# Optimization experiments

Hardware: AMD Instinct MI355X
Metric: run time of the kernel (lower is better)

The kernel has to match this reference:

```python
import math
import jax, jax.numpy as jnp
import numpy as np

B, T, E, H = 1, 2048, 2048, 16
D = E // H // 2  # head_dim = 64
DEPTH = 12
LAMBDA_INIT = 0.8 - 0.6 * math.exp(-0.3 * DEPTH)
EPS = 1e-5
NEG = -1e30


def rotary_cos_sin(seqlen, dim):
    # matches flash-attn RotaryEmbedding: inv_freq over even indices, base 10000
    inv_freq = 1.0 / (10000.0 ** (jnp.arange(0, dim, 2, dtype=jnp.float32) / dim))
    t = jnp.arange(seqlen, dtype=jnp.float32)
    freqs = jnp.outer(t, inv_freq)  # [T, D/2]
    return jnp.cos(freqs), jnp.sin(freqs)


def apply_rotary_interleaved(x, cos, sin):
    # x: [B, T, nH, D]; rotate interleaved pairs (x0,x1),(x2,x3),...
    x1 = x[..., 0::2]
    x2 = x[..., 1::2]
    c = cos[None, :, None, :]
    s = sin[None, :, None, :]
    o1 = x1 * c - x2 * s
    o2 = x1 * s + x2 * c
    return jnp.stack([o1, o2], axis=-1).reshape(x.shape)


def causal_attn_pair(q, k, v1, v2, mask, scale):
    # q,k,v*: [B, T, H, D]; shared softmax over (q,k), applied to both v1 and v2
    s = jnp.einsum('bthd,bshd->bhts', q, k) * scale
    s = jnp.where(mask, s, NEG)
    a = jax.nn.softmax(s, axis=-1)
    o1 = jnp.einsum('bhts,bshd->bthd', a, v1)
    o2 = jnp.einsum('bhts,bshd->bthd', a, v2)
    return jnp.concatenate([o1, o2], axis=-1)  # [B, T, H, 2D]


def setup_inputs() -> dict:
    key = jax.random.key(0)
    ks = jax.random.split(key, 10)
    return {
        'query': jax.random.normal(ks[0], (B, T, E), dtype=jnp.float32),
        'Wq': jax.random.normal(ks[1], (E, E), dtype=jnp.float32) * 0.02,
        'Wk': jax.random.normal(ks[2], (E, E), dtype=jnp.float32) * 0.02,
        'Wv': jax.random.normal(ks[3], (E, E), dtype=jnp.float32) * 0.02,
        'Wout': jax.random.normal(ks[4], (E, E), dtype=jnp.float32) * 0.02,
        'lambda_q1': jax.random.normal(ks[5], (D,), dtype=jnp.float32) * 0.1,
        'lambda_k1': jax.random.normal(ks[6], (D,), dtype=jnp.float32) * 0.1,
        'lambda_q2': jax.random.normal(ks[7], (D,), dtype=jnp.float32) * 0.1,
        'lambda_k2': jax.random.normal(ks[8], (D,), dtype=jnp.float32) * 0.1,
        'rms_weight': jnp.ones((2 * D,), dtype=jnp.float32),
    }


def reference(query, Wq, Wk, Wv, Wout, lambda_q1, lambda_k1, lambda_q2, lambda_k2, rms_weight):
    bsz, tgt_len, embed_dim = query.shape
    cos, sin = rotary_cos_sin(tgt_len, D)
    scale = D ** (-0.5)
    mask = jnp.tril(jnp.ones((tgt_len, tgt_len), dtype=bool))[None, None]

    q = (query @ Wq).reshape(bsz, tgt_len, 2 * H, D)
    k = (query @ Wk).reshape(bsz, tgt_len, 2 * H, D)
    v = (query @ Wv).reshape(bsz, tgt_len, H, 2, D)

    q = apply_rotary_emb = apply_rotary_interleaved(q, cos, sin)
    k = apply_rotary_interleaved(k, cos, sin)

    q = q.reshape(bsz, tgt_len, H, 2, D)
    k = k.reshape(bsz, tgt_len, H, 2, D)
    q1, q2 = q[:, :, :, 0], q[:, :, :, 1]
    k1, k2 = k[:, :, :, 0], k[:, :, :, 1]
    v1, v2 = v[:, :, :, 0], v[:, :, :, 1]

    attn1 = causal_attn_pair(q1, k1, v1, v2, mask, scale)  # [B,T,H,2D]
    attn2 = causal_attn_pair(q2, k2, v1, v2, mask, scale)

    lambda_1 = jnp.exp(jnp.sum(lambda_q1 * lambda_k1))
    lambda_2 = jnp.exp(jnp.sum(lambda_q2 * lambda_k2))
    lambda_full = lambda_1 - lambda_2 + LAMBDA_INIT

    f1 = jnp.fft.rfft(attn1, axis=1)
    f2 = jnp.fft.rfft(attn2, axis=1)
    attn_freq = f1 - lambda_full * f2

    n_freq = attn_freq.shape[1]
    sigma = 0.3 / 2.0  # cutoff_ratio / 2, gaussian window
    x = jnp.linspace(0.0, 1.0, n_freq)
    filt = jnp.exp(-0.5 * (x / sigma) ** 2)
    attn_freq = attn_freq * filt[None, :, None, None]

    attn = jnp.fft.irfft(attn_freq, n=tgt_len, axis=1)  # [B,T,H,2D]

    # RMSNorm over last dim (2*head_dim) with affine weight
    attn = attn * jax.lax.rsqrt(jnp.mean(attn * attn, axis=-1, keepdims=True) + EPS) * rms_weight
    attn = attn * (1.0 - LAMBDA_INIT)

    attn = attn.reshape(bsz, tgt_len, H * 2 * D)
    return attn @ Wout
```

## Files before the change

kernel.cpp:

```cpp
#include <hip/hip_runtime.h>
#include <math.h>

#define LAMBDA_INIT_F 0.7836057665316245f
#define ONE_MINUS_LI  0.2163942334683755f

typedef unsigned short ushort_t;
typedef unsigned int   uint32;
typedef unsigned long long u64;
typedef __attribute__((ext_vector_type(8))) short short8;
typedef __attribute__((ext_vector_type(4))) float f32x4;

__device__ __forceinline__ ushort_t f2bf(float f) {
    union { float f; uint32 u; } x; x.f = f;
    uint32 r = (x.u + 0x7fffu + ((x.u >> 16) & 1u)) >> 16;
    return (ushort_t)r;
}

__device__ __forceinline__ void gld16(ushort_t* lds, const ushort_t* g) {
    __builtin_amdgcn_global_load_lds(
        (const __attribute__((address_space(1))) uint32*)g,
        (__attribute__((address_space(3))) uint32*)lds,
        16, 0, 0);
}

__global__ __launch_bounds__(64) void lambda_kernel(
    const float* __restrict__ lq1, const float* __restrict__ lk1,
    const float* __restrict__ lq2, const float* __restrict__ lk2,
    float* __restrict__ lam)
{
    int l = threadIdx.x;
    float p1 = lq1[l] * lk1[l];
    float p2 = lq2[l] * lk2[l];
    for (int off = 32; off; off >>= 1) {
        p1 += __shfl_down(p1, off);
        p2 += __shfl_down(p2, off);
    }
    if (l == 0) lam[0] = expf(p1) - expf(p2) + LAMBDA_INIT_F;
}

__global__ __launch_bounds__(256) void gfilt_kernel(float* __restrict__ g)
{
    __shared__ float red[4];
    const int j = blockIdx.x;
    int tau = j - 64;
    int ta = tau < 0 ? -tau : tau;
    const int tid = threadIdx.x;
    float acc = 0.0f;
    for (int k = tid; k <= 1024; k += 256) {
        float w = (k == 0 || k == 1024) ? 1.0f : 2.0f;
        float r = (float)k * (1.0f / 153.6f);
        float f = expf(-0.5f * r * r);
        int m = (k * ta) & 2047;
        float ang = (float)m * 3.0679615757712823e-3f;
        acc += w * f * cosf(ang);
    }
    for (int off = 32; off; off >>= 1) acc += __shfl_down(acc, off);
    if ((tid & 63) == 0) red[tid >> 6] = acc;
    __syncthreads();
    if (tid == 0)
        g[j] = (red[0] + red[1] + red[2] + red[3]) * (1.0f / 2048.0f);
}

__global__ __launch_bounds__(256) void rottab(float* __restrict__ ct, float* __restrict__ st)
{
    int id = blockIdx.x * 256 + threadIdx.x;
    int t = id >> 5, i = id & 31;
    double inv = exp(-0.28782313662425575 * (double)i);
    double a = (double)t * inv;
    ct[id] = (float)cos(a);
    st[id] = (float)sin(a);
}

__global__ __launch_bounds__(256) void cvt_bf16(const float* __restrict__ s, ushort_t* __restrict__ d)
{
    int i = (blockIdx.x * 256 + threadIdx.x) * 8;
    float4 a = *(const float4*)(s + i);
    float4 b = *(const float4*)(s + i + 4);
    uint4 pk;
    pk.x = (uint32)f2bf(a.x) | ((uint32)f2bf(a.y) << 16);
    pk.y = (uint32)f2bf(a.z) | ((uint32)f2bf(a.w) << 16);
    pk.z = (uint32)f2bf(b.x) | ((uint32)f2bf(b.y) << 16);
    pk.w = (uint32)f2bf(b.z) | ((uint32)f2bf(b.w) << 16);
    *(uint4*)(d + i) = pk;
}

__global__ __launch_bounds__(256) void wtrans(
    const float* __restrict__ Wq, const float* __restrict__ Wk,
    const float* __restrict__ Wv, const float* __restrict__ Wo,
    ushort_t* __restrict__ Tq, ushort_t* __restrict__ Tk,
    ushort_t* __restrict__ Tv, ushort_t* __restrict__ To)
{
    int z = blockIdx.z;
    const float* S = (z == 0) ? Wq : (z == 1) ? Wk : (z == 2) ? Wv : Wo;
    ushort_t* Dt = (z == 0) ? Tq : (z == 1) ? Tk : (z == 2) ? Tv : To;
    bool perm = (z < 2);
    __shared__ float Ls[64 * 65];
    const int tid = threadIdx.x;
    const int n0 = blockIdx.x * 64, k0 = blockIdx.y * 64;
    #pragma unroll
    for (int it = 0; it < 4; ++it) {
        int kk = it * 16 + (tid >> 4);
        int nn = (tid & 15) * 4;
        float4 v = *(const float4*)(S + (size_t)(k0 + kk) * 2048 + n0 + nn);
        Ls[(nn + 0) * 65 + kk] = v.x;
        Ls[(nn + 1) * 65 + kk] = v.y;
        Ls[(nn + 2) * 65 + kk] = v.z;
        Ls[(nn + 3) * 65 + kk] = v.w;
    }
    __syncthreads();
    int nl = tid >> 2, kc = (tid & 3) * 16;
    int ng = n0 + nl;
    int nd = perm ? ((ng & ~63) | ((ng & 1) << 5) | ((ng & 63) >> 1)) : ng;
    uint4 p0, p1;
    const float* row = Ls + nl * 65 + kc;
    p0.x = (uint32)f2bf(row[0])  | ((uint32)f2bf(row[1])  << 16);
    p0.y = (uint32)f2bf(row[2])  | ((uint32)f2bf(row[3])  << 16);
    p0.z = (uint32)f2bf(row[4])  | ((uint32)f2bf(row[5])  << 16);
    p0.w = (uint32)f2bf(row[6])  | ((uint32)f2bf(row[7])  << 16);
    p1.x = (uint32)f2bf(row[8])  | ((uint32)f2bf(row[9])  << 16);
    p1.y = (uint32)f2bf(row[10]) | ((uint32)f2bf(row[11]) << 16);
    p1.z = (uint32)f2bf(row[12]) | ((uint32)f2bf(row[13]) << 16);
    p1.w = (uint32)f2bf(row[14]) | ((uint32)f2bf(row[15]) << 16);
    *(uint4*)(Dt + (size_t)nd * 2048 + k0 + kc) = p0;
    *(uint4*)(Dt + (size_t)nd * 2048 + k0 + kc + 8) = p1;
}

#define SB()    __builtin_amdgcn_s_barrier()
#define LGKM0() asm volatile("s_waitcnt lgkmcnt(0)" ::: "memory")
#define VM6()   asm volatile("s_waitcnt vmcnt(6)" ::: "memory")

__device__ __forceinline__ void rdA(short8 af[8], const ushort_t* Ah, int rbase, int quad)
{
    #pragma unroll
    for (int m = 0; m < 4; ++m) {
        int r = rbase + m * 16;
        #pragma unroll
        for (int ks = 0; ks < 2; ++ks)
            af[m * 2 + ks] = *(const short8*)(Ah + r * 64 + ((ks * 4 + quad) ^ (r & 7)) * 8);
    }
}
__device__ __forceinline__ void rdB(short8 bf[4], const ushort_t* Bh, int rbase, int quad)
{
    #pragma unroll
    for (int n = 0; n < 2; ++n) {
        int r = rbase + n * 32;
        #pragma unroll
        for (int ks = 0; ks < 2; ++ks)
            bf[n * 2 + ks] = *(const short8*)(Bh + r * 64 + ((ks * 4 + quad) ^ (r & 7)) * 8);
    }
}
template<int QA, int QB>
__device__ __forceinline__ void mfma16(const short8 af[8], const short8 bf[4], f32x4 acc[8][4])
{
    __builtin_amdgcn_s_setprio(1);
    #pragma unroll
    for (int m = 0; m < 4; ++m)
        #pragma unroll
        for (int n = 0; n < 2; ++n)
            #pragma unroll
            for (int ks = 0; ks < 2; ++ks)
                acc[QA * 4 + m][QB * 2 + n] = __builtin_amdgcn_mfma_f32_16x16x32_bf16(
                    af[m * 2 + ks], bf[n * 2 + ks], acc[QA * 4 + m][QB * 2 + n], 0, 0, 0);
    __builtin_amdgcn_s_setprio(0);
}

__global__ __launch_bounds__(512, 2) void gemm_qkv(
    const ushort_t* __restrict__ A, const ushort_t* __restrict__ WT,
    ushort_t* __restrict__ q1, ushort_t* __restrict__ q2,
    ushort_t* __restrict__ k1, ushort_t* __restrict__ k2,
    ushort_t* __restrict__ v1T, ushort_t* __restrict__ v2T,
    const float* __restrict__ ctab, const float* __restrict__ stab)
{
    __shared__ ushort_t sA0h0[8192], sA0h1[8192], sA1h0[8192], sA1h1[8192];
    __shared__ ushort_t sB0h0[8192], sB0h1[8192], sB1h0[8192], sB1h1[8192];
    const int tid = threadIdx.x;
    const int w = tid >> 6, lane = tid & 63;
    const int quad = lane >> 4, l15 = lane & 15;
    const int wr = w >> 2, wc = w & 3;
    const int rb = blockIdx.y * 256, cbg = blockIdx.x * 256;
    const int rA = wr * 64 + l15;
    const int rB = (wc >> 1) * 64 + (wc & 1) * 16 + l15;
    const int cib = w * 128;

    auto stA = [&](ushort_t* buf, int ha, int tau) {
        #pragma unroll
        for (int u = 0; u < 2; ++u) {
            int ci = cib + u * 64 + lane;
            int row = ci >> 3, cc = (ci & 7) ^ (row & 7);
            gld16(buf + (cib + u * 64) * 8,
                  A + (size_t)(rb + ha * 128 + row) * 2048 + tau * 64 + cc * 8);
        }
    };
    auto stB = [&](ushort_t* buf, int hb, int tau) {
        #pragma unroll
        for (int u = 0; u < 2; ++u) {
            int ci = cib + u * 64 + lane;
            int row = ci >> 3, cc = (ci & 7) ^ (row & 7);
            gld16(buf + (cib + u * 64) * 8,
                  WT + (size_t)(cbg + hb * 128 + row) * 2048 + tau * 64 + cc * 8);
        }
    };

    stA(sA0h0, 0, 0); stA(sA0h1, 1, 0); stB(sB0h0, 0, 0); stB(sB0h1, 1, 0);
    stA(sA1h0, 0, 1); stA(sA1h1, 1, 1); stB(sB1h0, 0, 1);

    f32x4 acc[8][4];
    #pragma unroll
    for (int i = 0; i < 8; ++i)
        #pragma unroll
        for (int j = 0; j < 4; ++j) acc[i][j] = (f32x4)0.0f;
    short8 af[8], bf[4];

    VM6();
    SB();

    for (int it = 0; it < 16; ++it) {
        const int t = it * 2;
        const int t1 = t + 1;
        const int t2 = (t + 2 < 32) ? t + 2 : 31;
        const int t3 = (t + 3 < 32) ? t + 3 : 31;
        rdA(af, sA0h0, rA, quad); rdB(bf, sB0h0, rB, quad);
        stB(sB1h1, 1, t1);
        SB(); LGKM0(); mfma16<0, 0>(af, bf, acc); SB();
        rdB(bf, sB0h1, rB, quad);
        stA(sA0h0, 0, t2);
        SB(); LGKM0(); mfma16<0, 1>(af, bf, acc); SB();
        rdA(af, sA0h1, rA, quad); rdB(bf, sB0h0, rB, quad);
        SB(); LGKM0(); mfma16<1, 0>(af, bf, acc); SB();
        rdB(bf, sB0h1, rB, quad);
        stA(sA0h1, 1, t2); stB(sB0h0, 0, t2);
        VM6();
        SB(); LGKM0(); mfma16<1, 1>(af, bf, acc); SB();
        rdA(af, sA1h0, rA, quad); rdB(bf, sB1h0, rB, quad);
        stB(sB0h1, 1, t2);
        SB(); LGKM0(); mfma16<0, 0>(af, bf, acc); SB();
        rdB(bf, sB1h1, rB, quad);
        stA(sA1h0, 0, t3);
        SB(); LGKM0(); mfma16<0, 1>(af, bf, acc); SB();
        rdA(af, sA1h1, rA, quad); rdB(bf, sB1h0, rB, quad);
        SB(); LGKM0(); mfma16<1, 0>(af, bf, acc); SB();
        rdB(bf, sB1h1, rB, quad);
        stA(sA1h1, 1, t3); stB(sB1h0, 0, t3);
        VM6();
        SB(); LGKM0(); mfma16<1, 1>(af, bf, acc); SB();
    }

    const int region = cbg >> 11;
    const int nloc = cbg & 2047;
    if (region < 2) {
        ushort_t* b1 = region ? k1 : q1;
        ushort_t* b2 = region ? k2 : q2;
        const int i = (wc & 1) * 16 + l15;
        #pragma unroll
        for (int qb = 0; qb < 2; ++qb) {
            int head2 = (nloc >> 6) + qb * 2 + (wc >> 1);
            ushort_t* dst = ((head2 & 1) ? b2 : b1) + (size_t)(head2 >> 1) * 2048 * 64;
            #pragma unroll
            for (int mi = 0; mi < 8; ++mi)
                #pragma unroll
                for (int r = 0; r < 4; ++r) {
                    int t = rb + (mi >> 2) * 128 + wr * 64 + (mi & 3) * 16 + quad * 4 + r;
                    float c = ctab[t * 32 + i], s = stab[t * 32 + i];
                    float x1 = acc[mi][qb * 2 + 0][r], x2 = acc[mi][qb * 2 + 1][r];
                    dst[(size_t)t * 64 + i]      = f2bf(x1 * c - x2 * s);
                    dst[(size_t)t * 64 + 32 + i] = f2bf(x1 * s + x2 * c);
                }
        }
    } else {
        #pragma unroll
        for (int mi = 0; mi < 8; ++mi)
            #pragma unroll
            for (int nj = 0; nj < 4; ++nj) {
                int cg = nloc + (nj >> 1) * 128 + (wc >> 1) * 64 + (wc & 1) * 16
                       + (nj & 1) * 32 + l15;
                int hh = cg >> 7, pr = (cg >> 6) & 1, d = cg & 63;
                int tb = rb + (mi >> 2) * 128 + wr * 64 + (mi & 3) * 16 + quad * 4;
                ushort_t* dst = (pr ? v2T : v1T) + ((size_t)(hh * 64 + d)) * 2048 + tb;
                u64 pk = (u64)f2bf(acc[mi][nj][0])
                       | ((u64)f2bf(acc[mi][nj][1]) << 16)
                       | ((u64)f2bf(acc[mi][nj][2]) << 32)
                       | ((u64)f2bf(acc[mi][nj][3]) << 48);
                *(u64*)dst = pk;
            }
    }
}

#define PSTRIDE 88

__device__ __forceinline__ void attn_step(
    const ushort_t* __restrict__ Kb, const ushort_t* __restrict__ V1b,
    const ushort_t* __restrict__ V2b, ushort_t* __restrict__ pw,
    const short8* qb, f32x4* O, float& m_i, float& l_i,
    int quad, int l15, int row_l, bool diag)
{
    f32x4 s[4];
    #pragma unroll
    for (int j = 0; j < 4; ++j) s[j] = (f32x4)0.0f;
    #pragma unroll
    for (int ks = 0; ks < 2; ++ks)
        #pragma unroll
        for (int j = 0; j < 4; ++j) {
            int r = j * 16 + l15;
            short8 kf = *(const short8*)(Kb + r * 64 + ((ks * 4 + quad) ^ (r & 7)) * 8);
            s[j] = __builtin_amdgcn_mfma_f32_16x16x32_bf16(kf, qb[ks], s[j], 0, 0, 0);
        }
    float mx = -1e30f;
    #pragma unroll
    for (int j = 0; j < 4; ++j)
        #pragma unroll
        for (int r = 0; r < 4; ++r) {
            float v = s[j][r] * 0.125f;
            if (diag) {
                int kp = j * 16 + quad * 4 + r;
                v = (kp <= row_l) ? v : -1e30f;
            }
            s[j][r] = v;
            mx = fmaxf(mx, v);
        }
    mx = fmaxf(mx, __shfl_xor(mx, 16));
    mx = fmaxf(mx, __shfl_xor(mx, 32));
    float newm = fmaxf(m_i, mx);
    float alpha = __expf(m_i - newm);
    float sum = 0.0f;
    #pragma unroll
    for (int j = 0; j < 4; ++j) {
        float p0 = __expf(s[j][0] - newm);
        float p1 = __expf(s[j][1] - newm);
        float p2 = __expf(s[j][2] - newm);
        float p3 = __expf(s[j][3] - newm);
        sum += (p0 + p1) + (p2 + p3);
        u64 pk = (u64)f2bf(p0) | ((u64)f2bf(p1) << 16)
               | ((u64)f2bf(p2) << 32) | ((u64)f2bf(p3) << 48);
        *(u64*)(pw + l15 * PSTRIDE + j * 16 + quad * 4) = pk;
    }
    sum += __shfl_xor(sum, 16);
    sum += __shfl_xor(sum, 32);
    l_i = l_i * alpha + sum;
    m_i = newm;
    float av0 = __shfl(alpha, quad * 4 + 0);
    float av1 = __shfl(alpha, quad * 4 + 1);
    float av2 = __shfl(alpha, quad * 4 + 2);
    float av3 = __shfl(alpha, quad * 4 + 3);
    #pragma unroll
    for (int nt = 0; nt < 8; ++nt) {
        O[nt][0] *= av0; O[nt][1] *= av1; O[nt][2] *= av2; O[nt][3] *= av3;
    }
    #pragma unroll
    for (int ks = 0; ks < 2; ++ks) {
        short8 pf = *(const short8*)(pw + l15 * PSTRIDE + ks * 32 + quad * 8);
        #pragma unroll
        for (int nt = 0; nt < 8; ++nt) {
            const ushort_t* Vs = (nt < 4) ? V1b : V2b;
            int d = (nt & 3) * 16 + l15;
            short8 vf = *(const short8*)(Vs + d * 64 + ((ks * 4 + quad) ^ (d & 7)) * 8);
            O[nt] = __builtin_amdgcn_mfma_f32_16x16x32_bf16(pf, vf, O[nt], 0, 0, 0);
        }
    }
}

__global__ __launch_bounds__(512, 4) void attn_pipe(
    const ushort_t* __restrict__ q1, const ushort_t* __restrict__ k1,
    const ushort_t* __restrict__ q2, const ushort_t* __restrict__ k2,
    const ushort_t* __restrict__ v1T, const ushort_t* __restrict__ v2T,
    float* __restrict__ X, const float* __restrict__ lam_ptr)
{
    __shared__ ushort_t Tt[4][4096];
    __shared__ ushort_t Ps[8][16 * PSTRIDE];

    const int tid = threadIdx.x;
    const int w = tid >> 6, lane = tid & 63;
    const int quad = lane >> 4, l15 = lane & 15;
    const int pair = w >> 2, wl = w & 3;
    const int b = blockIdx.x;
    const int h = b & 15;
    const int x16 = (b & 255) >> 4;
    const int qt = (b < 256) ? (31 - x16) : x16;
    const float lam = lam_ptr[0];
    const int row_l = wl * 16 + l15;

    const ushort_t* k1h = k1 + (size_t)h * 2048 * 64;
    const ushort_t* k2h = k2 + (size_t)h * 2048 * 64;
    const ushort_t* v1h = v1T + (size_t)h * 64 * 2048;
    const ushort_t* v2h = v2T + (size_t)h * 64 * 2048;

    short8 qb[2];
    {
        const ushort_t* qp = (pair ? q2 : q1)
            + ((size_t)h * 2048 + qt * 64 + wl * 16 + l15) * 64 + quad * 8;
        qb[0] = *(const short8*)(qp);
        qb[1] = *(const short8*)(qp + 32);
    }

    const int ci = tid;
    const int srow = ci >> 3, scc = (ci & 7) ^ (srow & 7);
    const int koff = srow * 64 + scc * 8;
    const int voff = srow * 2048 + scc * 8;

    short8 sK1, sK2, sV1, sV2;

    sK1 = *(const short8*)(k1h + koff);
    sK2 = *(const short8*)(k2h + koff);
    sV1 = *(const short8*)(v1h + voff);
    sV2 = *(const short8*)(v2h + voff);
    *(short8*)(&Tt[0][ci * 8]) = sK1;
    *(short8*)(&Tt[1][ci * 8]) = sK2;
    *(short8*)(&Tt[2][ci * 8]) = sV1;
    *(short8*)(&Tt[3][ci * 8]) = sV2;
    __syncthreads();

    f32x4 O[8];
    #pragma unroll
    for (int i = 0; i < 8; ++i) O[i] = (f32x4)0.0f;
    float m_i = -1e30f, l_i = 0.0f;

    const ushort_t* Kb = Tt[pair];

    for (int kt = 0; kt <= qt; ++kt) {
        if (kt < qt) {
            int kb = (kt + 1) * 4096, vb = (kt + 1) * 64;
            sK1 = *(const short8*)(k1h + kb + koff);
            sK2 = *(const short8*)(k2h + kb + koff);
            sV1 = *(const short8*)(v1h + vb + voff);
            sV2 = *(const short8*)(v2h + vb + voff);
        }
        attn_step(Kb, Tt[2], Tt[3], &Ps[w][0], qb, O, m_i, l_i,
                  quad, l15, row_l, kt == qt);
        __syncthreads();
        if (kt < qt) {
            *(short8*)(&Tt[0][ci * 8]) = sK1;
            *(short8*)(&Tt[1][ci * 8]) = sK2;
            *(short8*)(&Tt[2][ci * 8]) = sV1;
            *(short8*)(&Tt[3][ci * 8]) = sV2;
            __syncthreads();
        }
    }

    float sc = pair ? lam : 1.0f;
    float rr0 = sc / __shfl(l_i, quad * 4 + 0);
    float rr1 = sc / __shfl(l_i, quad * 4 + 1);
    float rr2 = sc / __shfl(l_i, quad * 4 + 2);
    float rr3 = sc / __shfl(l_i, quad * 4 + 3);

    float* LX = (float*)&Tt[0][0];
    const int rbase = wl * 16 + quad * 4;
    if (pair) {
        #pragma unroll
        for (int nt = 0; nt < 8; ++nt) {
            int cb = nt * 16 + l15;
            LX[(rbase + 0) * 128 + cb] = O[nt][0] * rr0;
            LX[(rbase + 1) * 128 + cb] = O[nt][1] * rr1;
            LX[(rbase + 2) * 128 + cb] = O[nt][2] * rr2;
            LX[(rbase + 3) * 128 + cb] = O[nt][3] * rr3;
        }
    }
    __syncthreads();
    if (!pair) {
        int tb = qt * 64 + rbase;
        #pragma unroll
        for (int nt = 0; nt < 8; ++nt) {
            int cb = nt * 16 + l15;
            int col = h * 128 + cb;
            X[(size_t)(tb + 0) * 2048 + col] = O[nt][0] * rr0 - LX[(rbase + 0) * 128 + cb];
            X[(size_t)(tb + 1) * 2048 + col] = O[nt][1] * rr1 - LX[(rbase + 1) * 128 + cb];
            X[(size_t)(tb + 2) * 2048 + col] = O[nt][2] * rr2 - LX[(rbase + 2) * 128 + cb];
            X[(size_t)(tb + 3) * 2048 + col] = O[nt][3] * rr3 - LX[(rbase + 3) * 128 + cb];
        }
    }
}

__global__ __launch_bounds__(256) void conv_t(
    const float* __restrict__ X, const float* __restrict__ g, float* __restrict__ Y)
{
    __shared__ float Xs[192 * 64];
    __shared__ float gs[129];
    const int tid = threadIdx.x;
    const int c0 = blockIdx.x * 64, t0 = blockIdx.y * 64;
    const int c = tid & 63, tg = tid >> 6;
    for (int j = tg; j < 192; j += 4)
        Xs[j * 64 + c] = X[(size_t)((t0 - 64 + j) & 2047) * 2048 + c0 + c];
    if (tid < 129) gs[tid] = g[tid];
    __syncthreads();
    float accv[16];
    #pragma unroll
    for (int i = 0; i < 16; ++i) accv[i] = 0.0f;
    const int tl0 = tg * 16;
    for (int tap = 0; tap < 129; ++tap) {
        float gv = gs[tap];
        int base = (tl0 + 128 - tap) * 64 + c;
        #pragma unroll
        for (int i = 0; i < 16; ++i) accv[i] += gv * Xs[base + i * 64];
    }
    #pragma unroll
    for (int i = 0; i < 16; ++i)
        Y[(size_t)(t0 + tl0 + i) * 2048 + c0 + c] = accv[i];
}

__global__ __launch_bounds__(64) void rms_bf(
    const float* __restrict__ Y, const float* __restrict__ wgt, ushort_t* __restrict__ yb)
{
    int grp = blockIdx.x;
    int t = grp >> 4, hh = grp & 15, l = threadIdx.x;
    size_t base = (size_t)t * 2048 + hh * 128;
    float a = Y[base + l];
    float b = Y[base + 64 + l];
    float ss = a * a + b * b;
    for (int off = 32; off; off >>= 1) ss += __shfl_down(ss, off);
    ss = __shfl(ss, 0);
    float r = rsqrtf(ss * (1.0f / 128.0f) + 1e-5f) * ONE_MINUS_LI;
    yb[base + l]      = f2bf(a * r * wgt[l]);
    yb[base + 64 + l] = f2bf(b * r * wgt[64 + l]);
}

__global__ __launch_bounds__(256) void gemm_out(
    const ushort_t* __restrict__ A, const ushort_t* __restrict__ BT,
    float* __restrict__ C)
{
    __shared__ ushort_t As[4096];
    __shared__ ushort_t Bs[8192];
    const int tid = threadIdx.x;
    const int w = tid >> 6, lane = tid & 63;
    const int quad = lane >> 4, l15 = lane & 15;
    const int wr = w >> 1, wc = w & 1;
    const int rb = blockIdx.y * 64, cb = blockIdx.x * 128;

    f32x4 acc[2][4];
    #pragma unroll
    for (int i = 0; i < 2; ++i)
        #pragma unroll
        for (int j = 0; j < 4; ++j) acc[i][j] = (f32x4)0.0f;

    for (int k0 = 0; k0 < 2048; k0 += 64) {
        #pragma unroll
        for (int u = 0; u < 2; ++u) {
            int off = (w * 2 + u) * 512;
            int Lc = (off >> 3) + lane;
            int row = Lc >> 3, cc = (Lc & 7) ^ (row & 7);
            gld16(As + off, A + (size_t)(rb + row) * 2048 + k0 + cc * 8);
        }
        #pragma unroll
        for (int u = 0; u < 4; ++u) {
            int off = (w * 4 + u) * 512;
            int Lc = (off >> 3) + lane;
            int row = Lc >> 3, cc = (Lc & 7) ^ (row & 7);
            gld16(Bs + off, BT + (size_t)(cb + row) * 2048 + k0 + cc * 8);
        }
        __syncthreads();
        #pragma unroll
        for (int ks = 0; ks < 2; ++ks) {
            short8 af[2], bfr[4];
            #pragma unroll
            for (int mi = 0; mi < 2; ++mi) {
                int r = wr * 32 + mi * 16 + l15;
                af[mi] = *(const short8*)(As + r * 64 + ((ks * 4 + quad) ^ (r & 7)) * 8);
            }
            #pragma unroll
            for (int nj = 0; nj < 4; ++nj) {
                int r = wc * 64 + nj * 16 + l15;
                bfr[nj] = *(const short8*)(Bs + r * 64 + ((ks * 4 + quad) ^ (r & 7)) * 8);
            }
            #pragma unroll
            for (int mi = 0; mi < 2; ++mi)
                #pragma unroll
                for (int nj = 0; nj < 4; ++nj)
                    acc[mi][nj] = __builtin_amdgcn_mfma_f32_16x16x32_bf16(
                        af[mi], bfr[nj], acc[mi][nj], 0, 0, 0);
        }
        __syncthreads();
    }

    #pragma unroll
    for (int mi = 0; mi < 2; ++mi)
        #pragma unroll
        for (int nj = 0; nj < 4; ++nj) {
            int cg = cb + wc * 64 + nj * 16 + l15;
            #pragma unroll
            for (int r = 0; r < 4; ++r) {
                int t = rb + wr * 32 + mi * 16 + quad * 4 + r;
                C[(size_t)t * 2048 + cg] = acc[mi][nj][r];
            }
        }
}

extern "C" void kernel_launch(void* const* d_in, const int* in_sizes, int n_in,
                              void* d_out, int out_size, void* d_ws, size_t ws_size,
                              hipStream_t stream)
{
    const float* query = (const float*)d_in[0];
    const float* Wq    = (const float*)d_in[1];
    const float* Wk    = (const float*)d_in[2];
    const float* Wv    = (const float*)d_in[3];
    const float* Wout  = (const float*)d_in[4];
    const float* lq1   = (const float*)d_in[5];
    const float* lk1   = (const float*)d_in[6];
    const float* lq2   = (const float*)d_in[7];
    const float* lk2   = (const float*)d_in[8];
    const float* rmsw  = (const float*)d_in[9];
    float* out = (float*)d_out;

    const size_t MB = 1ull << 20;
    char* W = (char*)d_ws;
    ushort_t* WqT   = (ushort_t*)(W + 0 * MB);
    ushort_t* WkT   = (ushort_t*)(W + 8 * MB);
    ushort_t* WvT   = (ushort_t*)(W + 16 * MB);
    ushort_t* WoutT = (ushort_t*)(W + 24 * MB);
    ushort_t* qb    = (ushort_t*)(W + 32 * MB);
    ushort_t* q1    = (ushort_t*)(W + 40 * MB);
    ushort_t* q2    = (ushort_t*)(W + 44 * MB);
    ushort_t* k1    = (ushort_t*)(W + 48 * MB);
    ushort_t* k2    = (ushort_t*)(W + 52 * MB);
    ushort_t* v1T   = (ushort_t*)(W + 56 * MB);
    ushort_t* v2T   = (ushort_t*)(W + 60 * MB);
    float*    X     = (float*)   (W + 64 * MB);
    float*    Y     = (float*)   (W + 32 * MB);
    ushort_t* ybf   = (ushort_t*)(W + 48 * MB);
    float*    ctab  = (float*)   (W + 80 * MB);
    float*    stab  = (float*)   (W + 80 * MB + 256 * 1024);
    float*    gbuf  = (float*)   (W + 80 * MB + 512 * 1024);
    float*    lam   = (float*)   (W + 80 * MB + 520 * 1024);

    lambda_kernel<<<1, 64, 0, stream>>>(lq1, lk1, lq2, lk2, lam);
    gfilt_kernel<<<129, 256, 0, stream>>>(gbuf);
    rottab<<<256, 256, 0, stream>>>(ctab, stab);
    cvt_bf16<<<2048, 256, 0, stream>>>(query, qb);
    wtrans<<<dim3(32, 32, 4), 256, 0, stream>>>(Wq, Wk, Wv, Wout, WqT, WkT, WvT, WoutT);

    gemm_qkv<<<dim3(24, 8), 512, 0, stream>>>(qb, WqT, q1, q2, k1, k2, v1T, v2T, ctab, stab);

    attn_pipe<<<512, 512, 0, stream>>>(q1, k1, q2, k2, v1T, v2T, X, lam);

    conv_t<<<dim3(32, 32), 256, 0, stream>>>(X, gbuf, Y);
    rms_bf<<<32768, 64, 0, stream>>>(Y, rmsw, ybf);

    gemm_out<<<dim3(16, 32), 256, 0, stream>>>(ybf, WoutT, out);
}
```

Measured before the change: 326.7 us.

## Double-buffer MFMA fragments so LDS reads overlap matrix core work in QKV GEMM

The QKV projection GEMM main loop now keeps two sets of A and B register fragments, issuing LDS reads for the next sub-tile before the MFMAs of the current one. The explicit lgkmcnt(0) waits are removed in favour of sched_barrier fences, leaving the compiler to insert the waits. Several redundant fragment reloads are dropped because the same fragments are reused across sub-steps. This aims to hide LDS latency behind matrix core work, at the cost of more VGPRs. It also relies on the barrier ordering being correct now that reads of buffers later overwritten by async global-to-LDS loads are issued earlier.

Measured after the change: 364.6 us. +11.6%, slower.

```diff
diff --git a/kernel.cpp b/kernel.cpp
--- a/kernel.cpp
+++ b/kernel.cpp
@@ -125,9 +125,9 @@
     *(uint4*)(Dt + (size_t)nd * 2048 + k0 + kc + 8) = p1;
 }
 
-#define SB()    __builtin_amdgcn_s_barrier()
-#define LGKM0() asm volatile("s_waitcnt lgkmcnt(0)" ::: "memory")
-#define VM6()   asm volatile("s_waitcnt vmcnt(6)" ::: "memory")
+#define SB()     __builtin_amdgcn_s_barrier()
+#define SCHED0() __builtin_amdgcn_sched_barrier(0)
+#define VM6()    asm volatile("s_waitcnt vmcnt(6)" ::: "memory")
 
 __device__ __forceinline__ void rdA(short8 af[8], const ushort_t* Ah, int rbase, int quad)
 {
@@ -209,40 +209,44 @@
     for (int i = 0; i < 8; ++i)
         #pragma unroll
         for (int j = 0; j < 4; ++j) acc[i][j] = (f32x4)0.0f;
-    short8 af[8], bf[4];
+    short8 afc[8], afn[8], bf0[4], bf1[4];
 
     VM6();
     SB();
+    rdA(afc, sA0h0, rA, quad); rdB(bf0, sB0h0, rB, quad);
+    SCHED0();
 
     for (int it = 0; it < 16; ++it) {
         const int t = it * 2;
         const int t1 = t + 1;
         const int t2 = (t + 2 < 32) ? t + 2 : 31;
         const int t3 = (t + 3 < 32) ? t + 3 : 31;
-        rdA(af, sA0h0, rA, quad); rdB(bf, sB0h0, rB, quad);
+        rdB(bf1, sB0h1, rB, quad); SCHED0();
         stB(sB1h1, 1, t1);
-        SB(); LGKM0(); mfma16<0, 0>(af, bf, acc); SB();
-        rdB(bf, sB0h1, rB, quad);
+        SB(); mfma16<0, 0>(afc, bf0, acc); SB();
+        rdA(afn, sA0h1, rA, quad); SCHED0();
         stA(sA0h0, 0, t2);
-        SB(); LGKM0(); mfma16<0, 1>(af, bf, acc); SB();
-        rdA(af, sA0h1, rA, quad); rdB(bf, sB0h0, rB, quad);
-        SB(); LGKM0(); mfma16<1, 0>(af, bf, acc); SB();
-        rdB(bf, sB0h1, rB, quad);
+        SB(); mfma16<0, 1>(afc, bf1, acc); SB();
+        mfma16<1, 0>(afn, bf0, acc); SB();
         stA(sA0h1, 1, t2); stB(sB0h0, 0, t2);
         VM6();
-        SB(); LGKM0(); mfma16<1, 1>(af, bf, acc); SB();
-        rdA(af, sA1h0, rA, quad); rdB(bf, sB1h0, rB, quad);
+        SB();
+        rdA(afc, sA1h0, rA, quad); rdB(bf0, sB1h0, rB, quad);
+        SCHED0();
+        mfma16<1, 1>(afn, bf1, acc); SB();
+        rdB(bf1, sB1h1, rB, quad); SCHED0();
         stB(sB0h1, 1, t2);
-        SB(); LGKM0(); mfma16<0, 0>(af, bf, acc); SB();
-        rdB(bf, sB1h1, rB, quad);
+        SB(); mfma16<0, 0>(afc, bf0, acc); SB();
+        rdA(afn, sA1h1, rA, quad); SCHED0();
         stA(sA1h0, 0, t3);
-        SB(); LGKM0(); mfma16<0, 1>(af, bf, acc); SB();
-        rdA(af, sA1h1, rA, quad); rdB(bf, sB1h0, rB, quad);
-        SB(); LGKM0(); mfma16<1, 0>(af, bf, acc); SB();
-        rdB(bf, sB1h1, rB, quad);
+        SB(); mfma16<0, 1>(afc, bf1, acc); SB();
+        mfma16<1, 0>(afn, bf0, acc); SB();
         stA(sA1h1, 1, t3); stB(sB1h0, 0, t3);
         VM6();
-        SB(); LGKM0(); mfma16<1, 1>(af, bf, acc); SB();
+        SB();
+        rdA(afc, sA0h0, rA, quad); rdB(bf0, sB0h0, rB, quad);
+        SCHED0();
+        mfma16<1, 1>(afn, bf1, acc); SB();
     }
 
     const int region = cbg >> 11;
```

## Double-buffer K/V tiles in LDS and re-layout P scratch

Applied to the files above, without the earlier changes.

The attention kernel now keeps two LDS copies of the K1/K2/V1/V2 tiles and writes the next tile into the inactive buffer right after computing on the current one. This removes one of the two block-wide barriers per key tile. It also switches the per-wave P scratch from a padded row-stride layout to a layout indexed by (j, quad) that is read back as two 8-byte loads, aiming to reduce LDS bank conflicts. LDS use rises from about 32KB+22KB to 64KB+16KB per block, which may cut the number of resident blocks per CU below the launch bound of 4.

Result: faster. 319.2 us (-2.3%).

```diff
diff --git a/kernel.cpp b/kernel.cpp
--- a/kernel.cpp
+++ b/kernel.cpp
@@ -285,8 +285,6 @@
     }
 }
 
-#define PSTRIDE 88
-
 __device__ __forceinline__ void attn_step(
     const ushort_t* __restrict__ Kb, const ushort_t* __restrict__ V1b,
     const ushort_t* __restrict__ V2b, ushort_t* __restrict__ pw,
@@ -331,7 +329,7 @@
         sum += (p0 + p1) + (p2 + p3);
         u64 pk = (u64)f2bf(p0) | ((u64)f2bf(p1) << 16)
                | ((u64)f2bf(p2) << 32) | ((u64)f2bf(p3) << 48);
-        *(u64*)(pw + l15 * PSTRIDE + j * 16 + quad * 4) = pk;
+        *(u64*)(pw + (j * 4 + quad) * 64 + l15 * 4) = pk;
     }
     sum += __shfl_xor(sum, 16);
     sum += __shfl_xor(sum, 32);
@@ -347,7 +345,10 @@
     }
     #pragma unroll
     for (int ks = 0; ks < 2; ++ks) {
-        short8 pf = *(const short8*)(pw + l15 * PSTRIDE + ks * 32 + quad * 8);
+        union { u64 q[2]; short8 v; } pu;
+        pu.q[0] = *(const u64*)(pw + (8 * ks + 2 * quad + 0) * 64 + l15 * 4);
+        pu.q[1] = *(const u64*)(pw + (8 * ks + 2 * quad + 1) * 64 + l15 * 4);
+        short8 pf = pu.v;
         #pragma unroll
         for (int nt = 0; nt < 8; ++nt) {
             const ushort_t* Vs = (nt < 4) ? V1b : V2b;
@@ -364,8 +365,8 @@
     const ushort_t* __restrict__ v1T, const ushort_t* __restrict__ v2T,
     float* __restrict__ X, const float* __restrict__ lam_ptr)
 {
-    __shared__ ushort_t Tt[4][4096];
-    __shared__ ushort_t Ps[8][16 * PSTRIDE];
+    __shared__ ushort_t Tt[2][4][4096];
+    __shared__ ushort_t Ps[8][1024];
 
     const int tid = threadIdx.x;
     const int w = tid >> 6, lane = tid & 63;
@@ -402,10 +403,10 @@
     sK2 = *(const short8*)(k2h + koff);
     sV1 = *(const short8*)(v1h + voff);
     sV2 = *(const short8*)(v2h + voff);
-    *(short8*)(&Tt[0][ci * 8]) = sK1;
-    *(short8*)(&Tt[1][ci * 8]) = sK2;
-    *(short8*)(&Tt[2][ci * 8]) = sV1;
-    *(short8*)(&Tt[3][ci * 8]) = sV2;
+    *(short8*)(&Tt[0][0][ci * 8]) = sK1;
+    *(short8*)(&Tt[0][1][ci * 8]) = sK2;
+    *(short8*)(&Tt[0][2][ci * 8]) = sV1;
+    *(short8*)(&Tt[0][3][ci * 8]) = sV2;
     __syncthreads();
 
     f32x4 O[8];
@@ -413,9 +414,8 @@
     for (int i = 0; i < 8; ++i) O[i] = (f32x4)0.0f;
     float m_i = -1e30f, l_i = 0.0f;
 
-    const ushort_t* Kb = Tt[pair];
-
     for (int kt = 0; kt <= qt; ++kt) {
+        const int p = kt & 1;
         if (kt < qt) {
             int kb = (kt + 1) * 4096, vb = (kt + 1) * 64;
             sK1 = *(const short8*)(k1h + kb + koff);
@@ -423,16 +423,15 @@
             sV1 = *(const short8*)(v1h + vb + voff);
             sV2 = *(const short8*)(v2h + vb + voff);
         }
-        attn_step(Kb, Tt[2], Tt[3], &Ps[w][0], qb, O, m_i, l_i,
-                  quad, l15, row_l, kt == qt);
+        attn_step(&Tt[p][pair][0], &Tt[p][2][0], &Tt[p][3][0], &Ps[w][0],
+                  qb, O, m_i, l_i, quad, l15, row_l, kt == qt);
+        if (kt < qt) {
+            *(short8*)(&Tt[p ^ 1][0][ci * 8]) = sK1;
+            *(short8*)(&Tt[p ^ 1][1][ci * 8]) = sK2;
+            *(short8*)(&Tt[p ^ 1][2][ci * 8]) = sV1;
+            *(short8*)(&Tt[p ^ 1][3][ci * 8]) = sV2;
+        }
         __syncthreads();
-        if (kt < qt) {
-            *(short8*)(&Tt[0][ci * 8]) = sK1;
-            *(short8*)(&Tt[1][ci * 8]) = sK2;
-            *(short8*)(&Tt[2][ci * 8]) = sV1;
-            *(short8*)(&Tt[3][ci * 8]) = sV2;
-            __syncthreads();
-        }
     }
 
     float sc = pair ? lam : 1.0f;
@@ -441,7 +440,7 @@
     float rr2 = sc / __shfl(l_i, quad * 4 + 2);
     float rr3 = sc / __shfl(l_i, quad * 4 + 3);
 
-    float* LX = (float*)&Tt[0][0];
+    float* LX = (float*)&Tt[0][0][0];
     const int rbase = wl * 16 + quad * 4;
     if (pair) {
         #pragma unroll
```
